# Kernel optimization log

Hardware: AMD Instinct MI355X
Metric: run time of the kernel (lower is better)

## Reference

```python
import jax, jax.numpy as jnp
import numpy as np

IGNORE_LABEL = -100  # config.data.ignore_label


def setup_inputs() -> dict:
    key = jax.random.key(0)
    k1, k2 = jax.random.split(key)
    V, D = 100000, 128            # voxel_num, feature dim of s_3d_output.F
    B, NV, H, W = 2, 4, 240, 320  # batch, n_views, height, width
    features_3d = jax.random.normal(k1, (V, D), dtype=jnp.float32)
    # raycast kernel output: per-pixel voxel index, or ignore_label for misses.
    raw = jax.random.randint(k2, (B, NV, H, W), 0, V + V // 4)
    indexes_image = jnp.where(raw < V, raw, IGNORE_LABEL).astype(jnp.int32)
    return {"features_3d": features_3d, "indexes_image": indexes_image}


def reference(features_3d, indexes_image):
    V = features_3d.shape[0]
    idx = indexes_image.reshape(-1)              # [P] flattened pixel->voxel index
    valid = idx != IGNORE_LABEL                  # [P] hit mask
    safe = jnp.where(valid, idx, 0)              # clamp misses for gather safety
    # projected_features[p] = features_3d[idx[p]] if hit else 0
    projected = jnp.where(valid[:, None], features_3d[safe], 0.0)  # [P, D]
    # mapping3dto2d_num: number of pixels each voxel projects to
    mapping3dto2d_num = jax.ops.segment_sum(
        jnp.where(valid, 1, 0).astype(jnp.int32), safe, num_segments=V)
    return projected, indexes_image, mapping3dto2d_num
```

## Files before the change

kernel.cpp:

```cpp
#include <hip/hip_runtime.h>

#define IGNORE_LABEL (-100)

typedef float f32x4 __attribute__((ext_vector_type(4)));

__global__ void RaycastFeatures_42597485641917_kernel(
        const f32x4* __restrict__ feat,
        const int*   __restrict__ idx,
        f32x4*       __restrict__ proj,
        float*       __restrict__ idx_out,
        float*       __restrict__ counts,
        int P) {
    const int tid  = blockIdx.x * blockDim.x + threadIdx.x;
    const int lane = tid & 31;
    const int grp0 = tid >> 5;
    const int ngrp = (gridDim.x * blockDim.x) >> 5;

    for (int p = grp0; p < P; p += ngrp) {
        const int  v     = __builtin_nontemporal_load(&idx[p]);
        const bool valid = (v != IGNORE_LABEL);

        if (lane == 0) {
            __builtin_nontemporal_store((float)v, &idx_out[p]);
            if (valid) atomicAdd(&counts[v], 1.0f);
        }

        f32x4 val = (f32x4)(0.f);
        if (valid) val = feat[(size_t)v * 32 + lane];
        __builtin_nontemporal_store(val, &proj[(size_t)p * 32 + lane]);
    }
}

extern "C" void kernel_launch(void* const* d_in, const int* in_sizes, int n_in,
                              void* d_out, int out_size, void* d_ws, size_t ws_size,
                              hipStream_t stream) {
    const float* feat = (const float*)d_in[0];
    const int*   idx  = (const int*)d_in[1];

    const int D = 128;
    const int V = in_sizes[0] / D;
    const int P = in_sizes[1];

    float* out     = (float*)d_out;
    f32x4* proj    = (f32x4*)out;
    float* idx_out = out + (size_t)P * D;
    float* counts  = idx_out + P;

    (void)hipMemsetAsync(counts, 0, (size_t)V * sizeof(float), stream);

    const int block = 256;
    const int grid  = 2048;
    RaycastFeatures_42597485641917_kernel<<<grid, block, 0, stream>>>(
        (const f32x4*)feat, idx, proj, idx_out, counts, P);
}
```

Measured before the change: 121.4 us.

## Split counts pass and partition gather by voxel-range slices for cache locality

Moves the index copy and count atomics into a separate vectorized kernel. The gather kernel now gives each block one of 16 voxel-index slices: every wave scans pixel chunks and uses ballot and shuffle to gather only the pixels whose voxel falls in its slice. The aim is to keep each block's feature reads within a smaller, cache-resident range. In exchange, every chunk's index array is read 16 times, rows are handled one at a time per wave with 64-bit loads, and an extra launch is added.

Measured after the change: 156.2 us. 28.7% more time.

```diff
diff --git a/kernel.cpp b/kernel.cpp
--- a/kernel.cpp
+++ b/kernel.cpp
@@ -2,32 +2,71 @@
 
 #define IGNORE_LABEL (-100)
 
-typedef float f32x4 __attribute__((ext_vector_type(4)));
+typedef float f32x2 __attribute__((ext_vector_type(2)));
 
-__global__ void RaycastFeatures_42597485641917_kernel(
-        const f32x4* __restrict__ feat,
+#define NSLICE 16
+#define GRID3  2048
+#define BLK    256
+#define WPC    ((GRID3 / NSLICE) * (BLK / 64))
+
+__global__ void k_pass_counts(const int* __restrict__ idx,
+                              float* __restrict__ idx_out,
+                              float* __restrict__ counts,
+                              int P) {
+    const int p0 = (blockIdx.x * blockDim.x + threadIdx.x) * 4;
+    if (p0 + 3 < P) {
+        const int4 v = *(const int4*)(idx + p0);
+        float4 f; f.x = (float)v.x; f.y = (float)v.y; f.z = (float)v.z; f.w = (float)v.w;
+        *(float4*)(idx_out + p0) = f;
+        if (v.x != IGNORE_LABEL) atomicAdd(&counts[v.x], 1.0f);
+        if (v.y != IGNORE_LABEL) atomicAdd(&counts[v.y], 1.0f);
+        if (v.z != IGNORE_LABEL) atomicAdd(&counts[v.z], 1.0f);
+        if (v.w != IGNORE_LABEL) atomicAdd(&counts[v.w], 1.0f);
+    } else {
+        for (int p = p0; p < P; ++p) {
+            const int v = idx[p];
+            idx_out[p] = (float)v;
+            if (v != IGNORE_LABEL) atomicAdd(&counts[v], 1.0f);
+        }
+    }
+}
+
+__global__ __launch_bounds__(BLK) void k_gather(
+        const f32x2* __restrict__ feat2,
         const int*   __restrict__ idx,
-        f32x4*       __restrict__ proj,
-        float*       __restrict__ idx_out,
-        float*       __restrict__ counts,
-        int P) {
-    const int tid  = blockIdx.x * blockDim.x + threadIdx.x;
-    const int lane = tid & 31;
-    const int grp0 = tid >> 5;
-    const int ngrp = (gridDim.x * blockDim.x) >> 5;
+        f32x2*       __restrict__ proj2,
+        int P, int V) {
+    const int lane  = threadIdx.x & 63;
+    const int wid   = threadIdx.x >> 6;
+    const int slice = blockIdx.x & (NSLICE - 1);
+    const int rank  = (blockIdx.x >> 4) * (BLK / 64) + wid;
+    const int nchunk = (P + 63) >> 6;
+    const float rsl = (float)NSLICE / (float)V;
 
-    for (int p = grp0; p < P; p += ngrp) {
-        const int  v     = __builtin_nontemporal_load(&idx[p]);
-        const bool valid = (v != IGNORE_LABEL);
-
-        if (lane == 0) {
-            __builtin_nontemporal_store((float)v, &idx_out[p]);
-            if (valid) atomicAdd(&counts[v], 1.0f);
+    for (int c = rank; c < nchunk; c += WPC) {
+        const int p = (c << 6) + lane;
+        const int v = (p < P) ? idx[p] : IGNORE_LABEL;
+        bool match;
+        if (p >= P) {
+            match = false;
+        } else if (v == IGNORE_LABEL) {
+            match = ((c & (NSLICE - 1)) == slice);
+        } else {
+            int sl = (int)((float)v * rsl);
+            sl = sl > (NSLICE - 1) ? (NSLICE - 1) : sl;
+            match = (sl == slice);
         }
-
-        f32x4 val = (f32x4)(0.f);
-        if (valid) val = feat[(size_t)v * 32 + lane];
-        __builtin_nontemporal_store(val, &proj[(size_t)p * 32 + lane]);
+        unsigned long long m = __ballot(match);
+        while (m) {
+            const int i  = __ffsll(m) - 1;
+            m &= (m - 1);
+            const int vv = __shfl(v, i, 64);
+            const int pp = (c << 6) + i;
+            f32x2 val = (f32x2)(0.f);
+            if (vv != IGNORE_LABEL)
+                val = feat2[(size_t)vv * 64 + lane];
+            __builtin_nontemporal_store(val, &proj2[(size_t)pp * 64 + lane]);
+        }
     }
 }
 
@@ -42,14 +81,15 @@
     const int P = in_sizes[1];
 
     float* out     = (float*)d_out;
-    f32x4* proj    = (f32x4*)out;
     float* idx_out = out + (size_t)P * D;
     float* counts  = idx_out + P;
 
     (void)hipMemsetAsync(counts, 0, (size_t)V * sizeof(float), stream);
 
-    const int block = 256;
-    const int grid  = 2048;
-    RaycastFeatures_42597485641917_kernel<<<grid, block, 0, stream>>>(
-        (const f32x4*)feat, idx, proj, idx_out, counts, P);
+    const int blkA  = 256;
+    const int gridA = (P / 4 + blkA - 1) / blkA;
+    k_pass_counts<<<gridA, blkA, 0, stream>>>(idx, idx_out, counts, P);
+
+    k_gather<<<GRID3, BLK, 0, stream>>>(
+        (const f32x2*)feat, idx, (f32x2*)out, P, V);
 }
```

## Bucket pixels by voxel via counting sort and emit features per voxel

Applied to the files above, without the earlier changes.

Replaces the per-pixel gather with a multi-kernel pipeline: count hits per voxel with integer atomics, prefix-scan the counts into offsets, scatter pixel indices into per-voxel buckets, then have each wave load a voxel row once and write it to every pixel that maps to it, zeroing missed pixels separately. The intent is to read each feature row only once instead of once per hit pixel and to replace float atomics with int atomics. It adds four extra kernel launches, a workspace-backed bucket array, scattered output writes, and dropped nontemporal hints, while the feature table is small enough that the per-pixel gathers may already hit in cache. k_scan2 only sums up to 128 block totals, which is enough for the current voxel count.

Result: slower. 143.1 us (+17.9%).

```diff
diff --git a/kernel.cpp b/kernel.cpp
--- a/kernel.cpp
+++ b/kernel.cpp
@@ -2,32 +2,151 @@
 
 #define IGNORE_LABEL (-100)
 
+typedef float f32x2 __attribute__((ext_vector_type(2)));
 typedef float f32x4 __attribute__((ext_vector_type(4)));
 
-__global__ void RaycastFeatures_42597485641917_kernel(
-        const f32x4* __restrict__ feat,
+
+__global__ void k_count_pass(const int* __restrict__ idx,
+                             float* __restrict__ idx_out,
+                             int* __restrict__ cnt, int P) {
+    const int p0 = (blockIdx.x * blockDim.x + threadIdx.x) * 4;
+    if (p0 + 3 < P) {
+        const int4 v = *(const int4*)(idx + p0);
+        float4 f; f.x = (float)v.x; f.y = (float)v.y; f.z = (float)v.z; f.w = (float)v.w;
+        *(float4*)(idx_out + p0) = f;
+        if (v.x != IGNORE_LABEL) atomicAdd(&cnt[v.x], 1);
+        if (v.y != IGNORE_LABEL) atomicAdd(&cnt[v.y], 1);
+        if (v.z != IGNORE_LABEL) atomicAdd(&cnt[v.z], 1);
+        if (v.w != IGNORE_LABEL) atomicAdd(&cnt[v.w], 1);
+    } else {
+        for (int p = p0; p < P && p >= 0; ++p) {
+            const int v = idx[p];
+            idx_out[p] = (float)v;
+            if (v != IGNORE_LABEL) atomicAdd(&cnt[v], 1);
+        }
+    }
+}
+
+__global__ __launch_bounds__(1024) void k_scan1(const int* __restrict__ cnt,
+                                                int* __restrict__ blockSums, int V) {
+    __shared__ int s[1024];
+    const int t = threadIdx.x;
+    const int g = blockIdx.x * 1024 + t;
+    s[t] = (g < V) ? cnt[g] : 0;
+    __syncthreads();
+    for (int d = 512; d > 0; d >>= 1) {
+        if (t < d) s[t] += s[t + d];
+        __syncthreads();
+    }
+    if (t == 0) blockSums[blockIdx.x] = s[0];
+}
+
+__global__ __launch_bounds__(1024) void k_scan2(const int* __restrict__ cnt,
+                                                const int* __restrict__ blockSums,
+                                                int* __restrict__ offsets,
+                                                int* __restrict__ cursor, int V) {
+    __shared__ int s[1024];
+    __shared__ int bsum[128];
+    const int t = threadIdx.x;
+    const int b = blockIdx.x;
+    const int g = b * 1024 + t;
+    const int x = (g < V) ? cnt[g] : 0;
+    s[t] = x;
+    if (t < 128) bsum[t] = (t < b) ? blockSums[t] : 0;
+    __syncthreads();
+    for (int d = 64; d > 0; d >>= 1) {
+        if (t < d) bsum[t] += bsum[t + d];
+        __syncthreads();
+    }
+    for (int d = 1; d < 1024; d <<= 1) {
+        int v_ = (t >= d) ? s[t - d] : 0;
+        __syncthreads();
+        s[t] += v_;
+        __syncthreads();
+    }
+    if (g < V) {
+        const int excl = bsum[0] + s[t] - x;
+        offsets[g] = excl;
+        cursor[g]  = excl;
+    }
+}
+
+__global__ void k_scatter(const int* __restrict__ idx,
+                          int* __restrict__ cursor,
+                          int* __restrict__ bucket, int P) {
+    const int p = blockIdx.x * blockDim.x + threadIdx.x;
+    if (p < P) {
+        const int v = idx[p];
+        if (v != IGNORE_LABEL) {
+            const int pos = atomicAdd(&cursor[v], 1);
+            bucket[pos] = p;
+        }
+    }
+}
+
+__global__ __launch_bounds__(256) void k_emit(
+        const f32x2* __restrict__ feat2,
         const int*   __restrict__ idx,
-        f32x4*       __restrict__ proj,
-        float*       __restrict__ idx_out,
-        float*       __restrict__ counts,
-        int P) {
+        const int*   __restrict__ cnt,
+        const int*   __restrict__ offsets,
+        const int*   __restrict__ bucket,
+        f32x2*       __restrict__ proj2,
+        float*       __restrict__ counts_f,
+        int P, int V) {
+    const int lane   = threadIdx.x & 63;
+    const int wid    = (blockIdx.x * blockDim.x + threadIdx.x) >> 6;
+    const int nwaves = (gridDim.x * blockDim.x) >> 6;
+
+    for (int v = wid; v < V; v += nwaves) {
+        const int n   = cnt[v];
+        const int off = offsets[v];
+        if (lane == 0) counts_f[v] = (float)n;
+        const f32x2 row = feat2[(size_t)v * 64 + lane];
+        for (int base = 0; base < n; base += 64) {
+            const int rem = n - base;
+            const int pix = (lane < rem) ? bucket[off + base + lane] : 0;
+            const int kmax = rem < 64 ? rem : 64;
+            for (int k = 0; k < kmax; ++k) {
+                const int p = __shfl(pix, k, 64);
+                proj2[(size_t)p * 64 + lane] = row;
+            }
+        }
+    }
+
+    const int nchunk = (P + 63) >> 6;
+    for (int c = wid; c < nchunk; c += nwaves) {
+        const int p = (c << 6) + lane;
+        const bool inval = (p < P) && (idx[p] == IGNORE_LABEL);
+        unsigned long long m = __ballot(inval);
+        while (m) {
+            const int i = __ffsll(m) - 1;
+            m &= (m - 1);
+            const int pp = (c << 6) + i;
+            proj2[(size_t)pp * 64 + lane] = (f32x2)(0.f);
+        }
+    }
+}
+
+__global__ void k_fallback(const f32x4* __restrict__ feat,
+                           const int* __restrict__ idx,
+                           f32x4* __restrict__ proj,
+                           float* __restrict__ idx_out,
+                           float* __restrict__ counts, int P) {
     const int tid  = blockIdx.x * blockDim.x + threadIdx.x;
     const int lane = tid & 31;
     const int grp0 = tid >> 5;
     const int ngrp = (gridDim.x * blockDim.x) >> 5;
-
     for (int p = grp0; p < P; p += ngrp) {
-        const int  v     = __builtin_nontemporal_load(&idx[p]);
+        const int v = idx[p];
         const bool valid = (v != IGNORE_LABEL);
-
+        const int s = valid ? v : 0;
+        f32x4 a = feat[(size_t)s * 32 + lane];
+        if (!valid) a = (f32x4)(0.f);
+        proj[(size_t)p * 32 + lane] = a;
         if (lane == 0) {
-            __builtin_nontemporal_store((float)v, &idx_out[p]);
+            idx_out[p] = (float)v;
             if (valid) atomicAdd(&counts[v], 1.0f);
         }
-
-        f32x4 val = (f32x4)(0.f);
-        if (valid) val = feat[(size_t)v * 32 + lane];
-        __builtin_nontemporal_store(val, &proj[(size_t)p * 32 + lane]);
     }
 }
 
@@ -42,14 +161,30 @@
     const int P = in_sizes[1];
 
     float* out     = (float*)d_out;
-    f32x4* proj    = (f32x4*)out;
     float* idx_out = out + (size_t)P * D;
     float* counts  = idx_out + P;
 
-    (void)hipMemsetAsync(counts, 0, (size_t)V * sizeof(float), stream);
+    const size_t need = (size_t)4 * V * 3 + 4096 + (size_t)4 * P;
+    if (ws_size < need) {
+        (void)hipMemsetAsync(counts, 0, (size_t)V * sizeof(float), stream);
+        k_fallback<<<2048, 256, 0, stream>>>((const f32x4*)feat, idx,
+                                             (f32x4*)out, idx_out, counts, P);
+        return;
+    }
 
-    const int block = 256;
-    const int grid  = 2048;
-    RaycastFeatures_42597485641917_kernel<<<grid, block, 0, stream>>>(
-        (const f32x4*)feat, idx, proj, idx_out, counts, P);
+    int* cnt       = (int*)d_ws;
+    int* offsets   = cnt + V;
+    int* blockSums = offsets + V;
+    int* cursor    = blockSums + 1024;
+    int* bucket    = cursor + V;
+
+    const int nScanBlk = (V + 1023) / 1024;
+
+    (void)hipMemsetAsync(cnt, 0, (size_t)V * sizeof(int), stream);
+    k_count_pass<<<(P / 4 + 255) / 256, 256, 0, stream>>>(idx, idx_out, cnt, P);
+    k_scan1<<<nScanBlk, 1024, 0, stream>>>(cnt, blockSums, V);
+    k_scan2<<<nScanBlk, 1024, 0, stream>>>(cnt, blockSums, offsets, cursor, V);
+    k_scatter<<<(P + 255) / 256, 256, 0, stream>>>(idx, cursor, bucket, P);
+    k_emit<<<2048, 256, 0, stream>>>((const f32x2*)feat, idx, cnt, offsets, bucket,
+                                     (f32x2*)out, counts, P, V);
 }
```
